# Performance work log

Hardware: AMD Instinct MI355X
Metric: run time of the kernel (lower is better)

## Reference

```python
import jax, jax.numpy as jnp
import numpy as np

B, IN, H = 4096, 1024, 2048


def setup_inputs() -> dict:
    key = jax.random.key(0)
    k1, k2, k3, k4 = jax.random.split(key, 4)
    x = jax.random.normal(k1, (B, IN), dtype=jnp.float32)
    h_prev = jax.random.normal(k2, (B, H), dtype=jnp.float32)
    c_prev = jax.random.normal(k3, (B, H), dtype=jnp.float32)
    # Fused weight for the 5 gate Linears (Wf, Wi, Wc, Wo, We), columns stacked.
    # Scaled like PyTorch Linear default init (~uniform(-1/sqrt(fan_in))).
    W = jax.random.normal(k4, (IN + H, 5 * H), dtype=jnp.float32) / jnp.sqrt(jnp.float32(IN + H))
    b = jnp.zeros((5 * H,), dtype=jnp.float32)
    return {"x": x, "h_prev": h_prev, "c_prev": c_prev, "W": W, "b": b}


def reference(x, h_prev, c_prev, W, b):
    combined = jnp.concatenate([x, h_prev], axis=1)          # [B, IN+H]
    z = combined @ W + b                                      # [B, 5H] single fused GEMM
    f, i, c_hat, o, e = jnp.split(z, 5, axis=1)
    ft = jax.nn.sigmoid(f)
    it = jax.nn.sigmoid(i)
    ct_hat = jnp.tanh(c_hat)
    ot = jax.nn.sigmoid(o)
    et = jax.nn.sigmoid(e)
    ct = ft * c_prev + it * ct_hat
    ht = ot * jnp.tanh(ct)
    ht = et * jnp.exp(ht) + (1.0 - et) * ht
    return ht, ct
```

## Files before the change

kernel.cpp:

```cpp
#include <hip/hip_runtime.h>
#include <hip/hip_bf16.h>
#include <stdint.h>

#define B_  4096
#define IN_ 1024
#define H_  2048
#define K_  (IN_ + H_)
#define N_  (5 * H_)

#define BM 128
#define BN 128
#define BK 32

typedef __attribute__((ext_vector_type(8))) short   short8;
typedef __attribute__((ext_vector_type(4))) float   f32x4;
typedef __attribute__((ext_vector_type(8))) unsigned short ushort8;

__device__ __forceinline__ unsigned short f2bf(float f) {
  union { float f; unsigned u; } cv; cv.f = f;
  unsigned u = cv.u;
  u += 0x7fffu + ((u >> 16) & 1u);
  return (unsigned short)(u >> 16);
}

__device__ __forceinline__ float bf2f(unsigned short s) {
  union { unsigned u; float f; } cv; cv.u = ((unsigned)s) << 16;
  return cv.f;
}

__device__ __forceinline__ void async16(const unsigned short* g, unsigned short* l) {
  __builtin_amdgcn_global_load_lds(
      (const __attribute__((address_space(1))) unsigned int*)g,
      (__attribute__((address_space(3))) unsigned int*)(void*)l,
      16, 0, 0);
}

__device__ __forceinline__ float fsig(float x) {
  return __builtin_amdgcn_rcpf(1.f + __expf(-x));
}
__device__ __forceinline__ float ftanh(float x) {
  return 1.f - 2.f * __builtin_amdgcn_rcpf(__expf(2.f * x) + 1.f);
}

__global__ void build_combined(const float* __restrict__ x,
                               const float* __restrict__ h,
                               unsigned short* __restrict__ out) {
  const int row = blockIdx.x;
  const float4* xr = (const float4*)(x + (size_t)row * IN_);
  const float4* hr = (const float4*)(h + (size_t)row * H_);
  uint2* orow = (uint2*)(out + (size_t)row * K_);
  for (int c = threadIdx.x; c < K_ / 4; c += 256) {
    float4 v = (c < IN_ / 4) ? xr[c] : hr[c - IN_ / 4];
    uint2 p;
    p.x = (unsigned)f2bf(v.x) | ((unsigned)f2bf(v.y) << 16);
    p.y = (unsigned)f2bf(v.z) | ((unsigned)f2bf(v.w) << 16);
    orow[c] = p;
  }
}

__global__ __launch_bounds__(256) void transpose_convert(
    const float* __restrict__ W, unsigned short* __restrict__ Wt) {
  __shared__ float tile[64][65];
  const int n0 = blockIdx.x * 64;
  const int k0 = blockIdx.y * 64;
  const int t  = threadIdx.x;

  const int lrow = t >> 2;
  #pragma unroll
  for (int i = 0; i < 4; ++i) {
    const int col4 = i * 4 + (t & 3);
    const float4 v = *(const float4*)&W[(size_t)(k0 + lrow) * N_ + n0 + col4 * 4];
    float* dst = &tile[lrow][col4 * 4];
    dst[0] = v.x; dst[1] = v.y; dst[2] = v.z; dst[3] = v.w;
  }
  __syncthreads();

  #pragma unroll
  for (int i = 0; i < 2; ++i) {
    const int c2 = t + i * 256;
    const int nn = c2 >> 3;
    const int kc = (c2 & 7) * 8;
    ushort8 p;
    #pragma unroll
    for (int u = 0; u < 8; ++u) p[u] = f2bf(tile[kc + u][nn]);
    *(ushort8*)&Wt[(size_t)(n0 + nn) * K_ + k0 + kc] = p;
  }
}

__global__ __launch_bounds__(256) void gemm_z(
    const unsigned short* __restrict__ A,
    const unsigned short* __restrict__ Bt,
    unsigned short* __restrict__ Z)
{
  __shared__ unsigned short As[BM * BK];
  __shared__ unsigned short Bs[BN * BK];

  const int tid  = threadIdx.x;
  const int wave = tid >> 6;
  const int lane = tid & 63;
  const int quad = lane >> 4;
  const int lr   = lane & 15;

  const int ntiles = N_ / BN;
  const int tile_n = blockIdx.x % ntiles;
  const int tile_m = blockIdx.x / ntiles;

  const int wm = (wave >> 1) * 64;
  const int wn = (wave & 1) * 64;

  f32x4 acc[4][4];
  #pragma unroll
  for (int i = 0; i < 4; ++i)
    #pragma unroll
    for (int j = 0; j < 4; ++j)
      acc[i][j] = (f32x4){0.f, 0.f, 0.f, 0.f};

  const int srow = wave * 32 + (lane >> 2);
  const int scol = (((lane & 3) ^ ((lane >> 3) & 3))) * 8;
  const unsigned short* aP = A  + ((size_t)tile_m * BM + srow) * K_ + scol;
  const unsigned short* bP = Bt + ((size_t)tile_n * BN + srow) * K_ + scol;
  unsigned short* aL0 = &As[(wave * 32)      * BK];
  unsigned short* aL1 = &As[(wave * 32 + 16) * BK];
  unsigned short* bL0 = &Bs[(wave * 32)      * BK];
  unsigned short* bL1 = &Bs[(wave * 32 + 16) * BK];
  const size_t k16 = (size_t)16 * K_;

  const int rslot = (quad ^ ((lr >> 1) & 3)) * 8;

  for (int k0 = 0; k0 < K_; k0 += BK) {
    async16(aP + k0,       aL0);
    async16(aP + k0 + k16, aL1);
    async16(bP + k0,       bL0);
    async16(bP + k0 + k16, bL1);
    __syncthreads();

    short8 af[4], bf[4];
    #pragma unroll
    for (int mi = 0; mi < 4; ++mi)
      af[mi] = *(const short8*)&As[(wm + mi * 16 + lr) * BK + rslot];
    #pragma unroll
    for (int ni = 0; ni < 4; ++ni)
      bf[ni] = *(const short8*)&Bs[(wn + ni * 16 + lr) * BK + rslot];

    #pragma unroll
    for (int mi = 0; mi < 4; ++mi)
      #pragma unroll
      for (int ni = 0; ni < 4; ++ni)
        acc[mi][ni] = __builtin_amdgcn_mfma_f32_16x16x32_bf16(
            af[mi], bf[ni], acc[mi][ni], 0, 0, 0);

    __syncthreads();
  }

  const size_t colbase = (size_t)tile_n * BN + wn + lr;
  #pragma unroll
  for (int mi = 0; mi < 4; ++mi) {
    #pragma unroll
    for (int r = 0; r < 4; ++r) {
      const size_t row = (size_t)tile_m * BM + wm + mi * 16 + quad * 4 + r;
      unsigned short* zp = Z + row * N_ + colbase;
      #pragma unroll
      for (int ni = 0; ni < 4; ++ni)
        zp[ni * 16] = f2bf(acc[mi][ni][r]);
    }
  }
}

__global__ __launch_bounds__(256) void epilogue(
    const unsigned short* __restrict__ Z,
    const float* __restrict__ c_prev,
    const float* __restrict__ b,
    float* __restrict__ out) {
  const int idx2 = blockIdx.x * 256 + threadIdx.x;
  const int r  = idx2 >> 10;
  const int j  = (idx2 & 1023) * 2;
  const unsigned short* zr = Z + (size_t)r * N_ + j;

  unsigned zg[5];
  float2 bg[5];
  #pragma unroll
  for (int g = 0; g < 5; ++g) {
    zg[g] = *(const unsigned*)(zr + g * H_);
    bg[g] = *(const float2*)(b + g * H_ + j);
  }
  const float2 cp = *(const float2*)(c_prev + (size_t)r * H_ + j);

  float ht[2], ct[2];
  #pragma unroll
  for (int u = 0; u < 2; ++u) {
    const float zf = bf2f((unsigned short)(zg[0] >> (16 * u))) + (u ? bg[0].y : bg[0].x);
    const float zi = bf2f((unsigned short)(zg[1] >> (16 * u))) + (u ? bg[1].y : bg[1].x);
    const float zc = bf2f((unsigned short)(zg[2] >> (16 * u))) + (u ? bg[2].y : bg[2].x);
    const float zo = bf2f((unsigned short)(zg[3] >> (16 * u))) + (u ? bg[3].y : bg[3].x);
    const float ze = bf2f((unsigned short)(zg[4] >> (16 * u))) + (u ? bg[4].y : bg[4].x);

    const float ft = fsig(zf);
    const float it = fsig(zi);
    const float ch = ftanh(zc);
    const float ot = fsig(zo);
    const float et = fsig(ze);

    const float c0 = u ? cp.y : cp.x;
    const float cn = ft * c0 + it * ch;
    const float th = ftanh(cn);
    float hn = ot * th;
    hn = et * __expf(hn) + (1.f - et) * hn;
    ht[u] = hn; ct[u] = cn;
  }

  float2* o1 = (float2*)(out + (size_t)r * H_ + j);
  float2* o2 = (float2*)(out + (size_t)B_ * H_ + (size_t)r * H_ + j);
  *o1 = make_float2(ht[0], ht[1]);
  *o2 = make_float2(ct[0], ct[1]);
}

extern "C" void kernel_launch(void* const* d_in, const int* in_sizes, int n_in,
                              void* d_out, int out_size, void* d_ws, size_t ws_size,
                              hipStream_t stream) {
  const float* x = (const float*)d_in[0];
  const float* h = (const float*)d_in[1];
  const float* c = (const float*)d_in[2];
  const float* W = (const float*)d_in[3];
  const float* b = (const float*)d_in[4];
  float* out = (float*)d_out;

  char* ws = (char*)d_ws;
  unsigned short* combined = (unsigned short*)ws;
  unsigned short* Wt = (unsigned short*)(ws + (size_t)25165824);
  unsigned short* Z  = (unsigned short*)(ws + (size_t)25165824 + 62914560);

  build_combined<<<B_, 256, 0, stream>>>(x, h, combined);
  transpose_convert<<<dim3(N_ / 64, K_ / 64), 256, 0, stream>>>(W, Wt);
  gemm_z<<<(B_ / BM) * (N_ / BN), 256, 0, stream>>>(combined, Wt, Z);
  epilogue<<<(B_ * H_) / 2 / 256, 256, 0, stream>>>(Z, c, b, out);
}
```

Measured before the change: 583.5 us.

## Fuse LSTM gate epilogue into GEMM by tiling across all five gates

The GEMM now computes, per block, a 128x32 column slice for each of the five gates (160 effective columns), so the gate nonlinearities and the cell/hidden update run directly on the accumulators and write final fp32 outputs. This removes the bf16 Z intermediate write and read and the separate epilogue launch. The new tile shape changes B-tile loading to gather five strided row groups, and output stores are now scalar per lane, which may be less coalesced. The transpose kernel's load indexing is also reorganized so each row is read contiguously by 16 threads.

```diff
diff --git a/kernel.cpp b/kernel.cpp
--- a/kernel.cpp
+++ b/kernel.cpp
@@ -9,7 +9,7 @@
 #define N_  (5 * H_)
 
 #define BM 128
-#define BN 128
+#define BJ 32
 #define BK 32
 
 typedef __attribute__((ext_vector_type(8))) short   short8;
@@ -21,11 +21,6 @@
   unsigned u = cv.u;
   u += 0x7fffu + ((u >> 16) & 1u);
   return (unsigned short)(u >> 16);
-}
-
-__device__ __forceinline__ float bf2f(unsigned short s) {
-  union { unsigned u; float f; } cv; cv.u = ((unsigned)s) << 16;
-  return cv.f;
 }
 
 __device__ __forceinline__ void async16(const unsigned short* g, unsigned short* l) {
@@ -65,12 +60,13 @@
   const int k0 = blockIdx.y * 64;
   const int t  = threadIdx.x;
 
-  const int lrow = t >> 2;
+  const int r0 = t >> 4;
+  const int c4 = t & 15;
   #pragma unroll
   for (int i = 0; i < 4; ++i) {
-    const int col4 = i * 4 + (t & 3);
-    const float4 v = *(const float4*)&W[(size_t)(k0 + lrow) * N_ + n0 + col4 * 4];
-    float* dst = &tile[lrow][col4 * 4];
+    const int kk = i * 16 + r0;
+    const float4 v = *(const float4*)&W[(size_t)(k0 + kk) * N_ + n0 + c4 * 4];
+    float* dst = &tile[kk][c4 * 4];
     dst[0] = v.x; dst[1] = v.y; dst[2] = v.z; dst[3] = v.w;
   }
   __syncthreads();
@@ -87,13 +83,15 @@
   }
 }
 
-__global__ __launch_bounds__(256) void gemm_z(
+__global__ __launch_bounds__(256) void gemm_fused(
     const unsigned short* __restrict__ A,
     const unsigned short* __restrict__ Bt,
-    unsigned short* __restrict__ Z)
+    const float* __restrict__ c_prev,
+    const float* __restrict__ bias,
+    float* __restrict__ out)
 {
   __shared__ unsigned short As[BM * BK];
-  __shared__ unsigned short Bs[BN * BK];
+  __shared__ unsigned short Bs[5 * BJ * BK];
 
   const int tid  = threadIdx.x;
   const int wave = tid >> 6;
@@ -101,117 +99,83 @@
   const int quad = lane >> 4;
   const int lr   = lane & 15;
 
-  const int ntiles = N_ / BN;
-  const int tile_n = blockIdx.x % ntiles;
-  const int tile_m = blockIdx.x / ntiles;
+  const int tile_m = blockIdx.x >> 6;
+  const int tile_j = blockIdx.x & 63;
+  const int m0 = tile_m * BM;
+  const int j0 = tile_j * BJ;
 
-  const int wm = (wave >> 1) * 64;
-  const int wn = (wave & 1) * 64;
+  const int wm = (wave & 1) * 64;
+  const int wn = (wave >> 1) * 16;
 
-  f32x4 acc[4][4];
+  f32x4 acc[4][5];
   #pragma unroll
-  for (int i = 0; i < 4; ++i)
+  for (int mi = 0; mi < 4; ++mi)
     #pragma unroll
-    for (int j = 0; j < 4; ++j)
-      acc[i][j] = (f32x4){0.f, 0.f, 0.f, 0.f};
+    for (int g = 0; g < 5; ++g)
+      acc[mi][g] = (f32x4){0.f, 0.f, 0.f, 0.f};
 
-  const int srow = wave * 32 + (lane >> 2);
-  const int scol = (((lane & 3) ^ ((lane >> 3) & 3))) * 8;
-  const unsigned short* aP = A  + ((size_t)tile_m * BM + srow) * K_ + scol;
-  const unsigned short* bP = Bt + ((size_t)tile_n * BN + srow) * K_ + scol;
-  unsigned short* aL0 = &As[(wave * 32)      * BK];
-  unsigned short* aL1 = &As[(wave * 32 + 16) * BK];
-  unsigned short* bL0 = &Bs[(wave * 32)      * BK];
-  unsigned short* bL1 = &Bs[(wave * 32 + 16) * BK];
+  const int lrow4 = lane >> 2;
+  const int scol  = ((lane & 3) ^ ((lane >> 3) & 3)) * 8;
+  const unsigned short* aBase = A  + ((size_t)(m0 + lrow4)) * K_ + scol;
+  const unsigned short* bBase = Bt + ((size_t)(j0 + lrow4)) * K_ + scol;
   const size_t k16 = (size_t)16 * K_;
 
   const int rslot = (quad ^ ((lr >> 1) & 3)) * 8;
 
   for (int k0 = 0; k0 < K_; k0 += BK) {
-    async16(aP + k0,       aL0);
-    async16(aP + k0 + k16, aL1);
-    async16(bP + k0,       bL0);
-    async16(bP + k0 + k16, bL1);
+    async16(aBase + (size_t)(wave * 32) * K_ + k0,      &As[(wave * 32) * BK]);
+    async16(aBase + (size_t)(wave * 32) * K_ + k16 + k0,&As[(wave * 32 + 16) * BK]);
+    for (int c = wave; c < 10; c += 4) {
+      const size_t roff = (size_t)((c >> 1) * H_ + (c & 1) * 16) * K_;
+      async16(bBase + roff + k0, &Bs[(c * 16) * BK]);
+    }
     __syncthreads();
 
-    short8 af[4], bf[4];
+    short8 af[4], bf[5];
     #pragma unroll
     for (int mi = 0; mi < 4; ++mi)
       af[mi] = *(const short8*)&As[(wm + mi * 16 + lr) * BK + rslot];
     #pragma unroll
-    for (int ni = 0; ni < 4; ++ni)
-      bf[ni] = *(const short8*)&Bs[(wn + ni * 16 + lr) * BK + rslot];
+    for (int g = 0; g < 5; ++g)
+      bf[g] = *(const short8*)&Bs[(g * 32 + wn + lr) * BK + rslot];
 
     #pragma unroll
     for (int mi = 0; mi < 4; ++mi)
       #pragma unroll
-      for (int ni = 0; ni < 4; ++ni)
-        acc[mi][ni] = __builtin_amdgcn_mfma_f32_16x16x32_bf16(
-            af[mi], bf[ni], acc[mi][ni], 0, 0, 0);
+      for (int g = 0; g < 5; ++g)
+        acc[mi][g] = __builtin_amdgcn_mfma_f32_16x16x32_bf16(
+            af[mi], bf[g], acc[mi][g], 0, 0, 0);
 
     __syncthreads();
   }
 
-  const size_t colbase = (size_t)tile_n * BN + wn + lr;
+  const int col = j0 + wn + lr;
+  float bb[5];
+  #pragma unroll
+  for (int g = 0; g < 5; ++g) bb[g] = bias[g * H_ + col];
+
   #pragma unroll
   for (int mi = 0; mi < 4; ++mi) {
+    float cp[4];
+    #pragma unroll
+    for (int r = 0; r < 4; ++r)
+      cp[r] = c_prev[(size_t)(m0 + wm + mi * 16 + quad * 4 + r) * H_ + col];
     #pragma unroll
     for (int r = 0; r < 4; ++r) {
-      const size_t row = (size_t)tile_m * BM + wm + mi * 16 + quad * 4 + r;
-      unsigned short* zp = Z + row * N_ + colbase;
-      #pragma unroll
-      for (int ni = 0; ni < 4; ++ni)
-        zp[ni * 16] = f2bf(acc[mi][ni][r]);
+      const int row = m0 + wm + mi * 16 + quad * 4 + r;
+      const float ft = fsig(acc[mi][0][r] + bb[0]);
+      const float it = fsig(acc[mi][1][r] + bb[1]);
+      const float ch = ftanh(acc[mi][2][r] + bb[2]);
+      const float ot = fsig(acc[mi][3][r] + bb[3]);
+      const float et = fsig(acc[mi][4][r] + bb[4]);
+      const float ct = ft * cp[r] + it * ch;
+      const float th = ftanh(ct);
+      float ht = ot * th;
+      ht = et * __expf(ht) + (1.f - et) * ht;
+      out[(size_t)row * H_ + col] = ht;
+      out[(size_t)B_ * H_ + (size_t)row * H_ + col] = ct;
     }
   }
-}
-
-__global__ __launch_bounds__(256) void epilogue(
-    const unsigned short* __restrict__ Z,
-    const float* __restrict__ c_prev,
-    const float* __restrict__ b,
-    float* __restrict__ out) {
-  const int idx2 = blockIdx.x * 256 + threadIdx.x;
-  const int r  = idx2 >> 10;
-  const int j  = (idx2 & 1023) * 2;
-  const unsigned short* zr = Z + (size_t)r * N_ + j;
-
-  unsigned zg[5];
-  float2 bg[5];
-  #pragma unroll
-  for (int g = 0; g < 5; ++g) {
-    zg[g] = *(const unsigned*)(zr + g * H_);
-    bg[g] = *(const float2*)(b + g * H_ + j);
-  }
-  const float2 cp = *(const float2*)(c_prev + (size_t)r * H_ + j);
-
-  float ht[2], ct[2];
-  #pragma unroll
-  for (int u = 0; u < 2; ++u) {
-    const float zf = bf2f((unsigned short)(zg[0] >> (16 * u))) + (u ? bg[0].y : bg[0].x);
-    const float zi = bf2f((unsigned short)(zg[1] >> (16 * u))) + (u ? bg[1].y : bg[1].x);
-    const float zc = bf2f((unsigned short)(zg[2] >> (16 * u))) + (u ? bg[2].y : bg[2].x);
-    const float zo = bf2f((unsigned short)(zg[3] >> (16 * u))) + (u ? bg[3].y : bg[3].x);
-    const float ze = bf2f((unsigned short)(zg[4] >> (16 * u))) + (u ? bg[4].y : bg[4].x);
-
-    const float ft = fsig(zf);
-    const float it = fsig(zi);
-    const float ch = ftanh(zc);
-    const float ot = fsig(zo);
-    const float et = fsig(ze);
-
-    const float c0 = u ? cp.y : cp.x;
-    const float cn = ft * c0 + it * ch;
-    const float th = ftanh(cn);
-    float hn = ot * th;
-    hn = et * __expf(hn) + (1.f - et) * hn;
-    ht[u] = hn; ct[u] = cn;
-  }
-
-  float2* o1 = (float2*)(out + (size_t)r * H_ + j);
-  float2* o2 = (float2*)(out + (size_t)B_ * H_ + (size_t)r * H_ + j);
-  *o1 = make_float2(ht[0], ht[1]);
-  *o2 = make_float2(ct[0], ct[1]);
 }
 
 extern "C" void kernel_launch(void* const* d_in, const int* in_sizes, int n_in,
@@ -227,10 +191,8 @@
   char* ws = (char*)d_ws;
   unsigned short* combined = (unsigned short*)ws;
   unsigned short* Wt = (unsigned short*)(ws + (size_t)25165824);
-  unsigned short* Z  = (unsigned short*)(ws + (size_t)25165824 + 62914560);
 
   build_combined<<<B_, 256, 0, stream>>>(x, h, combined);
   transpose_convert<<<dim3(N_ / 64, K_ / 64), 256, 0, stream>>>(W, Wt);
-  gemm_z<<<(B_ / BM) * (N_ / BN), 256, 0, stream>>>(combined, Wt, Z);
-  epilogue<<<(B_ * H_) / 2 / 256, 256, 0, stream>>>(Z, c, b, out);
+  gemm_fused<<<(B_ / BM) * (H_ / BJ), 256, 0, stream>>>(combined, Wt, c, b, out);
 }
```

After: 565.0 us. 3.2% less time.
